# Kernel tuning notes

Hardware: AMD Instinct MI355X
Metric: run time of the kernel (lower is better)

## Reference

```python
import jax, jax.numpy as jnp
import numpy as np

B, C, L, H, K, STRIDE = 8, 512, 2048, 8, 3, 1
D = C // H                       # head dim = 64
LQ = (L - K) // STRIDE + 1       # 'valid' conv output length = 2046
LN_EPS = 1e-5


def setup_inputs() -> dict:
    key = jax.random.key(0)
    ks = jax.random.split(key, 6)
    std = np.sqrt(2.0 / (C + C // H))  # init: sqrt(2 / sum(param.shape[:2]))
    inp = {
        "input": jax.random.normal(ks[0], (B, C, L), dtype=jnp.float32),
        "init_weight": jax.random.normal(ks[1], (B, C, LQ), dtype=jnp.float32),
        "q_w": jax.random.normal(ks[2], (C, C // H, K), dtype=jnp.float32) * std,
        "k_w": jax.random.normal(ks[3], (C, C // H, K), dtype=jnp.float32) * std,
        "v_w": jax.random.normal(ks[4], (C, C // H, K), dtype=jnp.float32) * std,
        "gamma": jnp.ones((C,), dtype=jnp.float32),
        "beta": jnp.zeros((C,), dtype=jnp.float32),
        # causal-style additive mask (1 above diagonal -> attention -= 1e9*mask)
        "mask": jnp.triu(jnp.ones((LQ, LQ), dtype=jnp.float32), k=1),
    }
    return inp


def _gconv(x, w):
    # x: [B, C, L], w: [C_out, C_in/groups, K] (torch OIH layout)
    return jax.lax.conv_general_dilated(
        x, w, window_strides=(STRIDE,), padding="VALID",
        dimension_numbers=("NCH", "OIH", "NCH"), feature_group_count=H)


def reference(input, init_weight, q_w, k_w, v_w, gamma, beta, mask):
    # grouped-conv QKV projections: [B, C, LQ]
    q = _gconv(input, q_w).reshape(B, H, D, LQ)
    k = _gconv(input, k_w).reshape(B, H, D, LQ)
    v = _gconv(input, v_w).reshape(B, H, D, LQ)

    # scores: q^T k per head; NOTE: faithful scale is 1/sqrt(multihead_num)
    att = jnp.einsum("bhdq,bhdk->bhqk", q, k)
    att = att / jnp.sqrt(jnp.asarray(H, att.dtype))
    att = att - 1e9 * mask  # broadcast [LQ, LQ] over [B, H, LQ, LQ]
    att = jax.nn.softmax(att, axis=-1)
    # dropout with p=0.0 is the identity (drop_rate=0.0)

    o = jnp.einsum("bhqk,bhdk->bhqd", att, v)          # [B, H, LQ, D]
    o = o.transpose(0, 2, 1, 3).reshape(B, LQ, C)       # merge heads (head-major channels)

    feat = o + init_weight.transpose(0, 2, 1)           # residual, [B, LQ, C]
    mu = jnp.mean(feat, axis=-1, keepdims=True)
    var = jnp.var(feat, axis=-1, keepdims=True)
    feat = (feat - mu) / jnp.sqrt(var + LN_EPS) * gamma + beta
    return feat  # [B, LQ, C]
```

## Files before the change

kernel.cpp:

```cpp
#include <hip/hip_runtime.h>

#define LQN 2046
#define LL  2048
#define CC  512
#define DD  64

typedef float  f32x4 __attribute__((ext_vector_type(4)));
typedef float  f32x2 __attribute__((ext_vector_type(2)));
typedef __bf16 b16x8 __attribute__((ext_vector_type(8)));
typedef unsigned int u32x4 __attribute__((ext_vector_type(4)));
typedef unsigned int u32x2 __attribute__((ext_vector_type(2)));

static __device__ __forceinline__ unsigned short f2bf(float f) {
  union { float f; unsigned u; } v; v.f = f;
  return (unsigned short)((v.u + 0x7fffu + ((v.u >> 16) & 1u)) >> 16);
}

static __device__ __forceinline__ unsigned cvtpk(float lo, float hi) {
  unsigned r;
  asm("v_cvt_pk_bf16_f32 %0, %1, %2" : "=v"(r) : "v"(lo), "v"(hi));
  return r;
}

static __device__ __forceinline__ f32x4 mfma16(b16x8 a, b16x8 b, f32x4 c) {
  return __builtin_amdgcn_mfma_f32_16x16x32_bf16(a, b, c, 0, 0, 0);
}

static __device__ __forceinline__ void glds16(const unsigned short* g, unsigned short* l) {
  __builtin_amdgcn_global_load_lds(
      (const __attribute__((address_space(1))) unsigned int*)(g),
      (__attribute__((address_space(3))) unsigned int*)(l),
      16, 0, 0);
}

__global__ __launch_bounds__(256) void conv_qkv_kernel(
    const float* __restrict__ in, const float* __restrict__ qw,
    const float* __restrict__ kw, const float* __restrict__ vw,
    unsigned short* __restrict__ qo, unsigned short* __restrict__ ko,
    unsigned short* __restrict__ vo)
{
  __shared__ __align__(16) unsigned short inT[130 * 72];
  __shared__ __align__(16) unsigned short buf[128 * 72];

  const int tile = blockIdx.x, g = blockIdx.y, b = blockIdx.z;
  const int t0 = tile * 128;
  const int tid = threadIdx.x;
  const int lane = tid & 63;
  const int wv = tid >> 6;
  const int r0 = lane & 15, qh = lane >> 4;

  {
    const int ci = tid & 63, ch = tid >> 6;
    const float* src = in + ((size_t)(b * CC + g * 64 + ci)) * LL;
    #pragma unroll
    for (int i = 0; i < 8; ++i) {
      int t = ch * 32 + i * 4;
      f32x4 d = *(const f32x4*)(src + t0 + t);
      inT[(t + 0) * 72 + ci] = f2bf(d.x);
      inT[(t + 1) * 72 + ci] = f2bf(d.y);
      inT[(t + 2) * 72 + ci] = f2bf(d.z);
      inT[(t + 3) * 72 + ci] = f2bf(d.w);
    }
    if (ch == 0) {
      #pragma unroll
      for (int e = 0; e < 2; ++e) {
        int t = 128 + e;
        int tg = t0 + t; if (tg > LL - 1) tg = LL - 1;
        inT[t * 72 + ci] = f2bf(src[tg]);
      }
    }
  }
  __syncthreads();

  const float* wptr[3] = {qw, kw, vw};
  const f32x4 zero4 = {0.f, 0.f, 0.f, 0.f};

  for (int p = 0; p < 3; ++p) {
    b16x8 aW[6];
    {
      const float* wb = wptr[p] + (size_t)(g * 64 + wv * 16 + r0) * 192;
      #pragma unroll
      for (int kc = 0; kc < 6; ++kc) {
        const int ktap = kc >> 1;
        const int cib = (kc & 1) * 32 + qh * 8;
        union { b16x8 v; unsigned short u[8]; } fr;
        #pragma unroll
        for (int j = 0; j < 8; ++j)
          fr.u[j] = f2bf(wb[(cib + j) * 3 + ktap]);
        aW[kc] = fr.v;
      }
    }
    f32x4 acc[8];
    #pragma unroll
    for (int nt = 0; nt < 8; ++nt) acc[nt] = zero4;
    #pragma unroll
    for (int kc = 0; kc < 6; ++kc) {
      const int radd = kc >> 1;
      const int colh = (kc & 1) * 32 + qh * 8;
      #pragma unroll
      for (int nt = 0; nt < 8; ++nt) {
        const int trow = nt * 16 + r0 + radd;
        b16x8 bI = *(const b16x8*)&inT[trow * 72 + colh];
        acc[nt] = mfma16(aW[kc], bI, acc[nt]);
      }
    }
    __syncthreads();
    if (p < 2) {
      const float qscl = (p == 0) ? 0.51006979f : 1.0f;
      #pragma unroll
      for (int nt = 0; nt < 8; ++nt) {
        const int t = nt * 16 + r0;
        #pragma unroll
        for (int r = 0; r < 4; ++r)
          buf[t * 72 + wv * 16 + qh * 4 + r] = f2bf(acc[nt][r] * qscl);
      }
      __syncthreads();
      unsigned short* dst = (p == 0 ? qo : ko) +
          ((size_t)(b * 8 + g) * LQN + t0) * DD;
      #pragma unroll
      for (int it = 0; it < 4; ++it) {
        const int id = it * 256 + tid;
        const int t = id >> 3, c8 = id & 7;
        if (t0 + t < LQN)
          *(u32x4*)(dst + t * DD + c8 * 8) = *(const u32x4*)&buf[t * 72 + c8 * 8];
      }
    } else {
      #pragma unroll
      for (int nt = 0; nt < 8; ++nt) {
        const int t = nt * 16 + r0;
        #pragma unroll
        for (int r = 0; r < 4; ++r)
          buf[(wv * 16 + qh * 4 + r) * 136 + t] = f2bf(acc[nt][r]);
      }
      __syncthreads();
      unsigned short* dst = vo + ((size_t)(b * CC + g * 64)) * LL + t0;
      #pragma unroll
      for (int it = 0; it < 4; ++it) {
        const int id = it * 256 + tid;
        const int row = id >> 4, c16 = id & 15;
        *(u32x4*)(dst + (size_t)row * LL + c16 * 8) =
            *(const u32x4*)&buf[row * 136 + c16 * 8];
      }
    }
    __syncthreads();
  }
}

static __device__ __forceinline__ void attn_tile(
    const unsigned short* __restrict__ Kl, const unsigned short* __restrict__ Vl,
    unsigned short* __restrict__ Pl,
    bool diag, int wv, int r0, int qh,
    b16x8 aQ0, b16x8 aQ1,
    f32x4 (&o)[4], float& mrun, float& lrun)
{
  f32x4 s[4];
  #pragma unroll
  for (int nt = 0; nt < 4; ++nt) {
    const int krow = nt * 16 + r0;
    const unsigned short* kr = Kl + krow * 64;
    const int sw = krow & 7;
    b16x8 k0 = *(const b16x8*)(kr + ((qh ^ sw) * 8));
    b16x8 k1 = *(const b16x8*)(kr + (((4 + qh) ^ sw) * 8));
    f32x4 acc = {0.f, 0.f, 0.f, 0.f};
    acc = mfma16(k0, aQ0, acc);
    s[nt] = mfma16(k1, aQ1, acc);
  }
  if (diag) {
    const int rowl = wv * 16 + r0;
    #pragma unroll
    for (int nt = 0; nt < 4; ++nt) {
      #pragma unroll
      for (int rr = 0; rr < 4; ++rr)
        if (nt * 16 + qh * 4 + rr > rowl) s[nt][rr] = -1e30f;
    }
  }
  f32x4 m01, m23;
  #pragma unroll
  for (int rr = 0; rr < 4; ++rr) {
    m01[rr] = fmaxf(s[0][rr], s[1][rr]);
    m23[rr] = fmaxf(s[2][rr], s[3][rr]);
  }
  #pragma unroll
  for (int rr = 0; rr < 4; ++rr) m01[rr] = fmaxf(m01[rr], m23[rr]);
  float mt = fmaxf(fmaxf(m01[0], m01[1]), fmaxf(m01[2], m01[3]));
  mt = fmaxf(mt, __shfl_xor(mt, 16));
  mt = fmaxf(mt, __shfl_xor(mt, 32));
  const float mn = fmaxf(mrun, mt);
  const float corr = __builtin_amdgcn_exp2f(mrun - mn);
  mrun = mn;
  #pragma unroll
  for (int nt = 0; nt < 4; ++nt)
    #pragma unroll
    for (int rr = 0; rr < 4; ++rr)
      s[nt][rr] = __builtin_amdgcn_exp2f(s[nt][rr] - mn);
  f32x4 t01, t23;
  #pragma unroll
  for (int rr = 0; rr < 4; ++rr) {
    t01[rr] = s[0][rr] + s[1][rr];
    t23[rr] = s[2][rr] + s[3][rr];
  }
  #pragma unroll
  for (int rr = 0; rr < 4; ++rr) t01[rr] += t23[rr];
  float sum = (t01[0] + t01[1]) + (t01[2] + t01[3]);
  sum += __shfl_xor(sum, 16);
  sum += __shfl_xor(sum, 32);
  lrun = lrun * corr + sum;
  const int xr = r0 & 7;
  unsigned short* pw = Pl + r0 * 64 + (qh & 1) * 4;
  #pragma unroll
  for (int nt = 0; nt < 4; ++nt) {
    u32x2 w;
    w.x = cvtpk(s[nt][0], s[nt][1]);
    w.y = cvtpk(s[nt][2], s[nt][3]);
    *(u32x2*)(pw + (((nt * 2 + (qh >> 1)) ^ xr) * 8)) = w;
  }
  #pragma unroll
  for (int rr = 0; rr < 4; ++rr) {
    const float cq = __shfl(corr, qh * 4 + rr);
    o[0][rr] *= cq; o[1][rr] *= cq; o[2][rr] *= cq; o[3][rr] *= cq;
  }
  #pragma unroll
  for (int kc = 0; kc < 2; ++kc) {
    b16x8 aP = *(const b16x8*)(Pl + r0 * 64 + (((kc * 4 + qh) ^ xr) * 8));
    #pragma unroll
    for (int dt = 0; dt < 4; ++dt) {
      const int vrow = dt * 16 + r0;
      b16x8 bv = *(const b16x8*)(Vl + vrow * 64 + (((kc * 4 + qh) ^ (vrow & 7)) * 8));
      o[dt] = mfma16(aP, bv, o[dt]);
    }
  }
}

static __device__ __forceinline__ void issue_tile(
    const unsigned short*& kSrc, const unsigned short*& vSrc,
    unsigned short* kDst, unsigned short* vDst)
{
  glds16(kSrc,          kDst);
  glds16(kSrc + 8 * DD, kDst + 512);
  glds16(vSrc,          vDst);
  glds16(vSrc + 8 * LL, vDst + 512);
  kSrc += 64 * DD;
  vSrc += 64;
}

static __device__ __forceinline__ void attn_epilogue(
    unsigned short* smem, const float* __restrict__ initw,
    float* __restrict__ out, int b, int h, int qt,
    int tid, int wv, int r0, int qh,
    f32x4 (&o)[4], float lrun)
{
  __syncthreads();
  float* initL = (float*)smem;
  const int cc = tid >> 2, qgrp = (tid & 3) * 16;
  const float* src = initw + (size_t)(b * CC + h * 64 + cc) * LQN;
  #pragma unroll
  for (int u = 0; u < 8; ++u) {
    int col = qt * 64 + qgrp + u * 2;
    if (col > LQN - 2) col = LQN - 2;
    f32x2 d = *(const f32x2*)(src + col);
    initL[cc * 65 + qgrp + u * 2]     = d.x;
    initL[cc * 65 + qgrp + u * 2 + 1] = d.y;
  }
  __syncthreads();
  #pragma unroll
  for (int r = 0; r < 4; ++r) {
    const float lq = __shfl(lrun, qh * 4 + r);
    const int ql = wv * 16 + qh * 4 + r;
    const int qgl = qt * 64 + ql;
    if (qgl >= LQN) continue;
    const float invl = 1.0f / lq;
    float* dst = out + ((size_t)(b * LQN + qgl)) * CC + h * 64;
    #pragma unroll
    for (int dt = 0; dt < 4; ++dt)
      dst[dt * 16 + r0] = o[dt][r] * invl + initL[(dt * 16 + r0) * 65 + ql];
  }
}

__global__ __launch_bounds__(256) void attn_kernel(
    const unsigned short* __restrict__ qg, const unsigned short* __restrict__ kg,
    const unsigned short* __restrict__ vg, const float* __restrict__ initw,
    float* __restrict__ out)
{
  __shared__ __align__(16) unsigned short KV[2][8192];
  __shared__ __align__(16) unsigned short Pb[4][1024];

  const int pi = blockIdx.x;
  const int hi = 31 - pi, lo = pi;
  const int bh = blockIdx.y;
  const int b = bh >> 3, h = bh & 7;
  const int tid = threadIdx.x, lane = tid & 63, wv = tid >> 6;
  const int r0 = lane & 15, qh = lane >> 4;

  const size_t kqbase = (size_t)bh * LQN * DD;
  const size_t vbase  = ((size_t)(b * CC + h * 64)) * LL;

  const int l8 = lane >> 3, c8s = lane & 7;
  const int csw = c8s ^ l8;
  const unsigned short* kSrc = kg + kqbase + (size_t)(wv * 16 + l8) * DD + csw * 8;
  const unsigned short* vSrc = vg + vbase  + (size_t)(wv * 16 + l8) * LL + csw * 8;

  b16x8 aQ0h, aQ1h, aQ0l, aQ1l;
  {
    int qrow = hi * 64 + wv * 16 + r0; if (qrow > LQN - 1) qrow = LQN - 1;
    const unsigned short* qp = qg + kqbase + (size_t)qrow * DD;
    aQ0h = *(const b16x8*)(qp + qh * 8);
    aQ1h = *(const b16x8*)(qp + 32 + qh * 8);
    qrow = lo * 64 + wv * 16 + r0;
    qp = qg + kqbase + (size_t)qrow * DD;
    aQ0l = *(const b16x8*)(qp + qh * 8);
    aQ1l = *(const b16x8*)(qp + 32 + qh * 8);
  }

  const f32x4 zero4 = {0.f, 0.f, 0.f, 0.f};
  f32x4 oh[4], ol[4];
  float mh = -1e30f, ml = -1e30f, lh = 0.f, llr = 0.f;
  #pragma unroll
  for (int dt = 0; dt < 4; ++dt) { oh[dt] = zero4; ol[dt] = zero4; }

  int bi = 0;
  issue_tile(kSrc, vSrc, &KV[0][wv * 1024], &KV[0][4096 + wv * 1024]);
  for (int kt = 0; kt <= hi; ++kt) {
    __syncthreads();
    if (kt < hi)
      issue_tile(kSrc, vSrc, &KV[bi ^ 1][wv * 1024], &KV[bi ^ 1][4096 + wv * 1024]);
    attn_tile(&KV[bi][0], &KV[bi][4096], Pb[wv], kt == hi, wv, r0, qh,
              aQ0h, aQ1h, oh, mh, lh);
    if (kt <= lo)
      attn_tile(&KV[bi][0], &KV[bi][4096], Pb[wv], kt == lo, wv, r0, qh,
                aQ0l, aQ1l, ol, ml, llr);
    bi ^= 1;
  }

  attn_epilogue(&KV[0][0], initw, out, b, h, hi, tid, wv, r0, qh, oh, lh);
  attn_epilogue(&KV[0][0], initw, out, b, h, lo, tid, wv, r0, qh, ol, llr);
}

__global__ __launch_bounds__(256) void ln_kernel(
    const float* __restrict__ gamma, const float* __restrict__ beta,
    float* __restrict__ out)
{
  const int row = blockIdx.x * 4 + ((int)threadIdx.x >> 6);
  const int lane = threadIdx.x & 63;
  if (row >= 8 * LQN) return;
  float* p = out + (size_t)row * CC;
  f32x4 x0 = *(const f32x4*)(p + lane * 8);
  f32x4 x1 = *(const f32x4*)(p + lane * 8 + 4);
  float s  = x0.x + x0.y + x0.z + x0.w + x1.x + x1.y + x1.z + x1.w;
  float sq = x0.x*x0.x + x0.y*x0.y + x0.z*x0.z + x0.w*x0.w
           + x1.x*x1.x + x1.y*x1.y + x1.z*x1.z + x1.w*x1.w;
  #pragma unroll
  for (int mm = 1; mm <= 32; mm <<= 1) {
    s  += __shfl_xor(s, mm);
    sq += __shfl_xor(sq, mm);
  }
  const float mu = s * (1.f / 512.f);
  const float var = sq * (1.f / 512.f) - mu * mu;
  const float rstd = rsqrtf(var + 1e-5f);
  f32x4 g0 = *(const f32x4*)(gamma + lane * 8);
  f32x4 g1 = *(const f32x4*)(gamma + lane * 8 + 4);
  f32x4 b0 = *(const f32x4*)(beta + lane * 8);
  f32x4 b1 = *(const f32x4*)(beta + lane * 8 + 4);
  x0 = (x0 - mu) * rstd * g0 + b0;
  x1 = (x1 - mu) * rstd * g1 + b1;
  *(f32x4*)(p + lane * 8)     = x0;
  *(f32x4*)(p + lane * 8 + 4) = x1;
}

extern "C" void kernel_launch(void* const* d_in, const int* in_sizes, int n_in,
                              void* d_out, int out_size, void* d_ws, size_t ws_size,
                              hipStream_t stream)
{
  const float* input = (const float*)d_in[0];
  const float* initw = (const float*)d_in[1];
  const float* qw    = (const float*)d_in[2];
  const float* kw    = (const float*)d_in[3];
  const float* vw    = (const float*)d_in[4];
  const float* gamma = (const float*)d_in[5];
  const float* beta  = (const float*)d_in[6];
  float* outp = (float*)d_out;

  unsigned short* q = (unsigned short*)d_ws;
  unsigned short* k = q + (16u * 1024u * 1024u / 2u);
  unsigned short* v = q + (32u * 1024u * 1024u / 2u);

  hipLaunchKernelGGL(conv_qkv_kernel, dim3(16, 8, 8), dim3(256), 0, stream,
                     input, qw, kw, vw, q, k, v);
  hipLaunchKernelGGL(attn_kernel, dim3(16, 64), dim3(256), 0, stream,
                     q, k, v, initw, outp);
  hipLaunchKernelGGL(ln_kernel, dim3(4092), dim3(256), 0, stream,
                     gamma, beta, outp);
}
```

Baseline: 150.4 us.

## Fuse hi/lo query tiles per KV tile and skip rescale when max unchanged

Merges the two per-tile attention calls (paired hi and lo query blocks) into one routine, so K and V fragments are read from LDS once and shared by both query blocks' MFMAs. It also adds a wave-uniform check that skips the output rescale and correction exp when the running max did not grow. This cuts LDS traffic and gives the scheduler more independent MFMAs to interleave. In exchange it raises register pressure from two live score sets and adds a divergent-free branch.

```diff
diff --git a/kernel.cpp b/kernel.cpp
--- a/kernel.cpp
+++ b/kernel.cpp
@@ -146,14 +146,92 @@
   }
 }
 
-static __device__ __forceinline__ void attn_tile(
+static __device__ __forceinline__ void softmax16(
+    f32x4 (&s)[4], f32x4 (&o)[4], float& mrun, float& lrun, int qh)
+{
+  f32x4 m01, m23;
+  #pragma unroll
+  for (int rr = 0; rr < 4; ++rr) {
+    m01[rr] = fmaxf(s[0][rr], s[1][rr]);
+    m23[rr] = fmaxf(s[2][rr], s[3][rr]);
+  }
+  #pragma unroll
+  for (int rr = 0; rr < 4; ++rr) m01[rr] = fmaxf(m01[rr], m23[rr]);
+  float mt = fmaxf(fmaxf(m01[0], m01[1]), fmaxf(m01[2], m01[3]));
+  mt = fmaxf(mt, __shfl_xor(mt, 16));
+  mt = fmaxf(mt, __shfl_xor(mt, 32));
+
+  if (__all(mt <= mrun)) {
+    const float mn = mrun;
+    #pragma unroll
+    for (int nt = 0; nt < 4; ++nt)
+      #pragma unroll
+      for (int rr = 0; rr < 4; ++rr)
+        s[nt][rr] = __builtin_amdgcn_exp2f(s[nt][rr] - mn);
+    f32x4 t01, t23;
+    #pragma unroll
+    for (int rr = 0; rr < 4; ++rr) {
+      t01[rr] = s[0][rr] + s[1][rr];
+      t23[rr] = s[2][rr] + s[3][rr];
+    }
+    #pragma unroll
+    for (int rr = 0; rr < 4; ++rr) t01[rr] += t23[rr];
+    float sum = (t01[0] + t01[1]) + (t01[2] + t01[3]);
+    sum += __shfl_xor(sum, 16);
+    sum += __shfl_xor(sum, 32);
+    lrun += sum;
+  } else {
+    const float mn = fmaxf(mrun, mt);
+    const float corr = __builtin_amdgcn_exp2f(mrun - mn);
+    mrun = mn;
+    #pragma unroll
+    for (int nt = 0; nt < 4; ++nt)
+      #pragma unroll
+      for (int rr = 0; rr < 4; ++rr)
+        s[nt][rr] = __builtin_amdgcn_exp2f(s[nt][rr] - mn);
+    f32x4 t01, t23;
+    #pragma unroll
+    for (int rr = 0; rr < 4; ++rr) {
+      t01[rr] = s[0][rr] + s[1][rr];
+      t23[rr] = s[2][rr] + s[3][rr];
+    }
+    #pragma unroll
+    for (int rr = 0; rr < 4; ++rr) t01[rr] += t23[rr];
+    float sum = (t01[0] + t01[1]) + (t01[2] + t01[3]);
+    sum += __shfl_xor(sum, 16);
+    sum += __shfl_xor(sum, 32);
+    lrun = lrun * corr + sum;
+    #pragma unroll
+    for (int rr = 0; rr < 4; ++rr) {
+      const float cq = __shfl(corr, qh * 4 + rr);
+      o[0][rr] *= cq; o[1][rr] *= cq; o[2][rr] *= cq; o[3][rr] *= cq;
+    }
+  }
+}
+
+static __device__ __forceinline__ void pack_p(
+    const f32x4 (&s)[4], unsigned short* __restrict__ Pl, int r0, int qh)
+{
+  const int xr = r0 & 7;
+  unsigned short* pw = Pl + r0 * 64 + (qh & 1) * 4;
+  #pragma unroll
+  for (int nt = 0; nt < 4; ++nt) {
+    u32x2 w;
+    w.x = cvtpk(s[nt][0], s[nt][1]);
+    w.y = cvtpk(s[nt][2], s[nt][3]);
+    *(u32x2*)(pw + (((nt * 2 + (qh >> 1)) ^ xr) * 8)) = w;
+  }
+}
+
+static __device__ __forceinline__ void attn_tile2(
     const unsigned short* __restrict__ Kl, const unsigned short* __restrict__ Vl,
     unsigned short* __restrict__ Pl,
-    bool diag, int wv, int r0, int qh,
-    b16x8 aQ0, b16x8 aQ1,
-    f32x4 (&o)[4], float& mrun, float& lrun)
-{
-  f32x4 s[4];
+    bool diagH, bool loActive, bool diagL, int wv, int r0, int qh,
+    b16x8 aQ0h, b16x8 aQ1h, b16x8 aQ0l, b16x8 aQ1l,
+    f32x4 (&oh)[4], float& mh, float& lh,
+    f32x4 (&ol)[4], float& ml, float& ll)
+{
+  f32x4 sh[4], sl[4];
   #pragma unroll
   for (int nt = 0; nt < 4; ++nt) {
     const int krow = nt * 16 + r0;
@@ -161,72 +239,56 @@
     const int sw = krow & 7;
     b16x8 k0 = *(const b16x8*)(kr + ((qh ^ sw) * 8));
     b16x8 k1 = *(const b16x8*)(kr + (((4 + qh) ^ sw) * 8));
-    f32x4 acc = {0.f, 0.f, 0.f, 0.f};
-    acc = mfma16(k0, aQ0, acc);
-    s[nt] = mfma16(k1, aQ1, acc);
-  }
-  if (diag) {
+    f32x4 a0 = {0.f, 0.f, 0.f, 0.f};
+    a0 = mfma16(k0, aQ0h, a0);
+    sh[nt] = mfma16(k1, aQ1h, a0);
+    if (loActive) {
+      f32x4 a1 = {0.f, 0.f, 0.f, 0.f};
+      a1 = mfma16(k0, aQ0l, a1);
+      sl[nt] = mfma16(k1, aQ1l, a1);
+    }
+  }
+  if (diagH) {
     const int rowl = wv * 16 + r0;
     #pragma unroll
-    for (int nt = 0; nt < 4; ++nt) {
+    for (int nt = 0; nt < 4; ++nt)
       #pragma unroll
       for (int rr = 0; rr < 4; ++rr)
-        if (nt * 16 + qh * 4 + rr > rowl) s[nt][rr] = -1e30f;
-    }
-  }
-  f32x4 m01, m23;
-  #pragma unroll
-  for (int rr = 0; rr < 4; ++rr) {
-    m01[rr] = fmaxf(s[0][rr], s[1][rr]);
-    m23[rr] = fmaxf(s[2][rr], s[3][rr]);
-  }
-  #pragma unroll
-  for (int rr = 0; rr < 4; ++rr) m01[rr] = fmaxf(m01[rr], m23[rr]);
-  float mt = fmaxf(fmaxf(m01[0], m01[1]), fmaxf(m01[2], m01[3]));
-  mt = fmaxf(mt, __shfl_xor(mt, 16));
-  mt = fmaxf(mt, __shfl_xor(mt, 32));
-  const float mn = fmaxf(mrun, mt);
-  const float corr = __builtin_amdgcn_exp2f(mrun - mn);
-  mrun = mn;
-  #pragma unroll
-  for (int nt = 0; nt < 4; ++nt)
-    #pragma unroll
-    for (int rr = 0; rr < 4; ++rr)
-      s[nt][rr] = __builtin_amdgcn_exp2f(s[nt][rr] - mn);
-  f32x4 t01, t23;
-  #pragma unroll
-  for (int rr = 0; rr < 4; ++rr) {
-    t01[rr] = s[0][rr] + s[1][rr];
-    t23[rr] = s[2][rr] + s[3][rr];
-  }
-  #pragma unroll
-  for (int rr = 0; rr < 4; ++rr) t01[rr] += t23[rr];
-  float sum = (t01[0] + t01[1]) + (t01[2] + t01[3]);
-  sum += __shfl_xor(sum, 16);
-  sum += __shfl_xor(sum, 32);
-  lrun = lrun * corr + sum;
+        if (nt * 16 + qh * 4 + rr > rowl) sh[nt][rr] = -1e30f;
+  }
+  if (loActive && diagL) {
+    const int rowl = wv * 16 + r0;
+    #pragma unroll
+    for (int nt = 0; nt < 4; ++nt)
+      #pragma unroll
+      for (int rr = 0; rr < 4; ++rr)
+        if (nt * 16 + qh * 4 + rr > rowl) sl[nt][rr] = -1e30f;
+  }
+
   const int xr = r0 & 7;
-  unsigned short* pw = Pl + r0 * 64 + (qh & 1) * 4;
-  #pragma unroll
-  for (int nt = 0; nt < 4; ++nt) {
-    u32x2 w;
-    w.x = cvtpk(s[nt][0], s[nt][1]);
-    w.y = cvtpk(s[nt][2], s[nt][3]);
-    *(u32x2*)(pw + (((nt * 2 + (qh >> 1)) ^ xr) * 8)) = w;
-  }
-  #pragma unroll
-  for (int rr = 0; rr < 4; ++rr) {
-    const float cq = __shfl(corr, qh * 4 + rr);
-    o[0][rr] *= cq; o[1][rr] *= cq; o[2][rr] *= cq; o[3][rr] *= cq;
-  }
-  #pragma unroll
-  for (int kc = 0; kc < 2; ++kc) {
-    b16x8 aP = *(const b16x8*)(Pl + r0 * 64 + (((kc * 4 + qh) ^ xr) * 8));
-    #pragma unroll
-    for (int dt = 0; dt < 4; ++dt) {
-      const int vrow = dt * 16 + r0;
-      b16x8 bv = *(const b16x8*)(Vl + vrow * 64 + (((kc * 4 + qh) ^ (vrow & 7)) * 8));
-      o[dt] = mfma16(aP, bv, o[dt]);
+  softmax16(sh, oh, mh, lh, qh);
+  pack_p(sh, Pl, r0, qh);
+  b16x8 aPh0 = *(const b16x8*)(Pl + r0 * 64 + ((qh ^ xr) * 8));
+  b16x8 aPh1 = *(const b16x8*)(Pl + r0 * 64 + (((4 + qh) ^ xr) * 8));
+  b16x8 aPl0, aPl1;
+  if (loActive) {
+    softmax16(sl, ol, ml, ll, qh);
+    pack_p(sl, Pl, r0, qh);
+    aPl0 = *(const b16x8*)(Pl + r0 * 64 + ((qh ^ xr) * 8));
+    aPl1 = *(const b16x8*)(Pl + r0 * 64 + (((4 + qh) ^ xr) * 8));
+  }
+  #pragma unroll
+  for (int dt = 0; dt < 4; ++dt) {
+    const int vrow = dt * 16 + r0;
+    const unsigned short* vr = Vl + vrow * 64;
+    const int sw = vrow & 7;
+    b16x8 bv0 = *(const b16x8*)(vr + ((qh ^ sw) * 8));
+    b16x8 bv1 = *(const b16x8*)(vr + (((4 + qh) ^ sw) * 8));
+    oh[dt] = mfma16(aPh0, bv0, oh[dt]);
+    oh[dt] = mfma16(aPh1, bv1, oh[dt]);
+    if (loActive) {
+      ol[dt] = mfma16(aPl0, bv0, ol[dt]);
+      ol[dt] = mfma16(aPl1, bv1, ol[dt]);
     }
   }
 }
@@ -323,11 +385,9 @@
     __syncthreads();
     if (kt < hi)
       issue_tile(kSrc, vSrc, &KV[bi ^ 1][wv * 1024], &KV[bi ^ 1][4096 + wv * 1024]);
-    attn_tile(&KV[bi][0], &KV[bi][4096], Pb[wv], kt == hi, wv, r0, qh,
-              aQ0h, aQ1h, oh, mh, lh);
-    if (kt <= lo)
-      attn_tile(&KV[bi][0], &KV[bi][4096], Pb[wv], kt == lo, wv, r0, qh,
-                aQ0l, aQ1l, ol, ml, llr);
+    attn_tile2(&KV[bi][0], &KV[bi][4096], Pb[wv],
+               kt == hi, kt <= lo, kt == lo, wv, r0, qh,
+               aQ0h, aQ1h, aQ0l, aQ1l, oh, mh, lh, ol, ml, llr);
     bi ^= 1;
   }
 
```

New measurement: 167.2 us. +11.2%, slower.
